# Kernel optimization log

Measured on AMD Instinct MI355X. Metric: run time of the kernel, lower is better.

## Reference

```python
import jax, jax.numpy as jnp
import numpy as np


def setup_inputs() -> dict:
    key = jax.random.key(0)
    ks = jax.random.split(key, 6)
    T, n_vars, n_channels, hidden = 2048, 64, 256, 512
    # VarianceScaling(2.0,'fan_in','uniform') ~ uniform(-limit, limit), limit=sqrt(3*2/fan_in)
    limit = float(np.sqrt(3.0 * 2.0 / n_channels))
    return {
        "enriched_history": jax.random.normal(ks[0], (T, n_vars, n_channels), dtype=jnp.float32),
        "target_mask": jax.random.randint(ks[1], (n_vars,), 0, 2, dtype=jnp.int32),
        "intervention_mask": jax.random.randint(ks[2], (n_vars,), 0, 2, dtype=jnp.int32),
        "W_target": jax.random.uniform(ks[3], (n_channels, hidden), jnp.float32, -limit, limit),
        "b_target": jnp.zeros((hidden,), jnp.float32),
        "W_intervention": jax.random.uniform(ks[4], (n_channels, hidden), jnp.float32, -limit, limit),
        "b_intervention": jnp.zeros((hidden,), jnp.float32),
        "W_other": jax.random.uniform(ks[5], (n_channels, hidden), jnp.float32, -limit, limit),
        "b_other": jnp.zeros((hidden,), jnp.float32),
    }


def reference(enriched_history, target_mask, intervention_mask,
              W_target, b_target, W_intervention, b_intervention,
              W_other, b_other):
    T, n_vars, n_channels = enriched_history.shape
    tm = target_mask.astype(jnp.float32)                       # [n_vars]
    im = intervention_mask.astype(jnp.float32) * (1.0 - tm)    # exclusivity
    om = (1.0 - tm) * (1.0 - im)

    flat = enriched_history.reshape(T * n_vars, n_channels)    # [T*n_vars, C]
    proj_t = flat @ W_target + b_target                        # [T*n_vars, H]
    proj_i = flat @ W_intervention + b_intervention
    proj_o = flat @ W_other + b_other

    # Faithful to original: jnp.repeat(mask, T) -> each variable's flag repeated T times
    tm_flat = jnp.repeat(tm, T)
    im_flat = jnp.repeat(im, T)
    om_flat = jnp.repeat(om, T)

    combined = (proj_t * tm_flat[:, None]
                + proj_i * im_flat[:, None]
                + proj_o * om_flat[:, None])
    return combined.reshape(T, n_vars, -1)
```

## Files before the change

### kernel.cpp

```cpp
#include <hip/hip_runtime.h>

typedef float f32x4 __attribute__((ext_vector_type(4)));
typedef unsigned short u16x8 __attribute__((ext_vector_type(8)));
typedef __bf16 bf16x8 __attribute__((ext_vector_type(8)));
typedef __bf16 bf16x4 __attribute__((ext_vector_type(4)));

__global__ __launch_bounds__(256) void convert_w_kernel(
    const float* __restrict__ Wt_, const float* __restrict__ Wi_,
    const float* __restrict__ Wo_, unsigned short* __restrict__ out)
{
    __shared__ unsigned short tile[64][72];

    const int b    = blockIdx.x;
    const int role = b >> 5;
    const int kt   = (b & 31) >> 3;
    const int nt   = b & 7;
    const float* __restrict__ W = (role == 0) ? Wt_ : ((role == 1) ? Wi_ : Wo_);

    const int t  = threadIdx.x;
    const int r0 = t >> 4;
    const int c4 = (t & 15) << 2;

#pragma unroll
    for (int j = 0; j < 4; ++j) {
        const int kl = r0 + j * 16;
        f32x4 v = *(const f32x4*)(W + (size_t)(kt * 64 + kl) * 512 + nt * 64 + c4);
#pragma unroll
        for (int e = 0; e < 4; ++e)
            tile[c4 + e][kl] = __builtin_bit_cast(unsigned short, (__bf16)v[e]);
    }
    __syncthreads();

    const int cs = t & 7;
#pragma unroll
    for (int p = 0; p < 2; ++p) {
        const int r = (t >> 3) + p * 32;
        u16x8 v = *(const u16x8*)&tile[r][cs * 8];
        *(u16x8*)(out + (size_t)role * 512 * 256 +
                  (size_t)(nt * 64 + r) * 256 + kt * 64 + cs * 8) = v;
    }
}

__global__ __launch_bounds__(512, 4) void role_proj_kernel(
    const float* __restrict__ A,
    const int* __restrict__ tmask,
    const int* __restrict__ imask,
    const unsigned short* __restrict__ Wws,
    const float* __restrict__ bt, const float* __restrict__ bi,
    const float* __restrict__ bo,
    float* __restrict__ C)
{
    __shared__ __align__(16) unsigned char smem[32 * 1024];
    unsigned short* As = (unsigned short*)smem;

    const int tid = threadIdx.x;
    const int m0  = blockIdx.x * 64;

    const int mi   = blockIdx.x >> 5;
    const int role = tmask[mi] ? 0 : (imask[mi] ? 1 : 2);
    const unsigned short* __restrict__ W = Wws + (size_t)role * (512 * 256);
    const float* __restrict__ bias = (role == 0) ? bt : ((role == 1) ? bi : bo);

    const f32x4* abase = (const f32x4*)(A + (size_t)m0 * 256);
    f32x4 ld[8];
#pragma unroll
    for (int p = 0; p < 8; ++p)
        ld[p] = __builtin_nontemporal_load(abase + tid + 512 * p);
#pragma unroll
    for (int p = 0; p < 8; ++p) {
        const int u    = tid + 512 * p;
        const int row  = u >> 6;
        const int slot = ((u & 63) >> 1) ^ (row & 7);
        bf16x4 pk = { (__bf16)ld[p][0], (__bf16)ld[p][1],
                      (__bf16)ld[p][2], (__bf16)ld[p][3] };
        *(bf16x4*)(smem + row * 512 + slot * 16 + (u & 1) * 8) = pk;
    }
    __syncthreads();

    const int lane  = tid & 63;
    const int wid   = tid >> 6;
    const int l15   = lane & 15;
    const int l4    = lane >> 4;
    const int nbase = wid * 64;
    const int r7    = l15 & 7;

    const unsigned short* wp[4];
#pragma unroll
    for (int fn = 0; fn < 4; ++fn)
        wp[fn] = W + (size_t)(nbase + fn * 16 + l15) * 256 + l4 * 8;

    f32x4 acc[4][4] = {};

#pragma unroll 1
    for (int ks = 0; ks < 8; ++ks) {
        u16x8 bfr[4];
#pragma unroll
        for (int fn = 0; fn < 4; ++fn)
            bfr[fn] = *(const u16x8*)(wp[fn] + ks * 32);
        u16x8 afr[4];
#pragma unroll
        for (int fm = 0; fm < 4; ++fm) {
            const int row  = fm * 16 + l15;
            const int slot = (ks * 4 + l4) ^ r7;
            afr[fm] = *(const u16x8*)&As[row * 256 + slot * 8];
        }
#pragma unroll
        for (int fm = 0; fm < 4; ++fm) {
#pragma unroll
            for (int fn = 0; fn < 4; ++fn) {
                acc[fm][fn] = __builtin_amdgcn_mfma_f32_16x16x32_bf16(
                    __builtin_bit_cast(bf16x8, bfr[fn]),
                    __builtin_bit_cast(bf16x8, afr[fm]),
                    acc[fm][fn], 0, 0, 0);
            }
        }
    }

    __builtin_amdgcn_sched_barrier(0);
    __builtin_amdgcn_s_barrier();
    __builtin_amdgcn_sched_barrier(0);

    f32x4 bv[4];
#pragma unroll
    for (int fn = 0; fn < 4; ++fn)
        bv[fn] = *(const f32x4*)(bias + nbase + fn * 16 + l4 * 4);

#pragma unroll
    for (int p = 0; p < 4; ++p) {
#pragma unroll
        for (int fn = 0; fn < 4; ++fn) {
            const int chunk = (wid * 16 + fn * 4 + l4) ^ r7;
            *(f32x4*)(smem + l15 * 2048 + chunk * 16) = acc[p][fn] + bv[fn];
        }
        asm volatile("s_waitcnt lgkmcnt(0)" ::: "memory");
        __builtin_amdgcn_sched_barrier(0);
        __builtin_amdgcn_s_barrier();
        __builtin_amdgcn_sched_barrier(0);

#pragma unroll
        for (int q = 0; q < 4; ++q) {
            const int f4    = tid + 512 * q;
            const int row   = f4 >> 7;
            const int chunk = f4 & 127;
            f32x4 v = *(const f32x4*)(smem + row * 2048 + (chunk ^ (row & 7)) * 16);
            __builtin_nontemporal_store(
                v, (f32x4*)(C + ((size_t)(m0 + p * 16 + row) << 9) + chunk * 4));
        }
        if (p < 3) {
            __builtin_amdgcn_sched_barrier(0);
            __builtin_amdgcn_s_barrier();
            __builtin_amdgcn_sched_barrier(0);
        }
    }
}

extern "C" void kernel_launch(void* const* d_in, const int* in_sizes, int n_in,
                              void* d_out, int out_size, void* d_ws, size_t ws_size,
                              hipStream_t stream) {
    const float* A   = (const float*)d_in[0];
    const int*   tm  = (const int*)d_in[1];
    const int*   im  = (const int*)d_in[2];
    const float* Wt_ = (const float*)d_in[3];
    const float* bt  = (const float*)d_in[4];
    const float* Wi_ = (const float*)d_in[5];
    const float* bi  = (const float*)d_in[6];
    const float* Wo_ = (const float*)d_in[7];
    const float* bo  = (const float*)d_in[8];

    unsigned short* Wws = (unsigned short*)d_ws;

    hipLaunchKernelGGL(convert_w_kernel, dim3(96), dim3(256),
                       0, stream, Wt_, Wi_, Wo_, Wws);

    hipLaunchKernelGGL(role_proj_kernel, dim3(2048), dim3(512),
                       0, stream, A, tm, im, Wws, bt, bi, bo, (float*)d_out);
}
```

Before: 123.2 us.

## Make projection blocks loop over four tiles with double-buffered A prefetch

Each block now processes four consecutive 64-row tiles instead of one, using a 2x32KB LDS double buffer. The next A tile's global loads are issued before the epilogue and converted into the other buffer afterwards, so input fetch overlaps with output writeback and MFMA work. The grid drops from 2048 to 512 blocks, and output stores become regular stores instead of nontemporal. The cost is doubled LDS per block, which limits how many blocks fit on a CU, plus extra barriers per iteration.

New measurement: 160.8 us. +30.5%, slower.

```diff
diff --git a/kernel.cpp b/kernel.cpp
--- a/kernel.cpp
+++ b/kernel.cpp
@@ -50,32 +50,15 @@
     const float* __restrict__ bo,
     float* __restrict__ C)
 {
-    __shared__ __align__(16) unsigned char smem[32 * 1024];
-    unsigned short* As = (unsigned short*)smem;
-
-    const int tid = threadIdx.x;
-    const int m0  = blockIdx.x * 64;
-
-    const int mi   = blockIdx.x >> 5;
+    __shared__ __align__(16) unsigned char smem[2][32 * 1024];
+
+    const int tid   = threadIdx.x;
+    const int tile0 = blockIdx.x * 4;
+
+    const int mi   = blockIdx.x >> 3;
     const int role = tmask[mi] ? 0 : (imask[mi] ? 1 : 2);
     const unsigned short* __restrict__ W = Wws + (size_t)role * (512 * 256);
     const float* __restrict__ bias = (role == 0) ? bt : ((role == 1) ? bi : bo);
-
-    const f32x4* abase = (const f32x4*)(A + (size_t)m0 * 256);
-    f32x4 ld[8];
-#pragma unroll
-    for (int p = 0; p < 8; ++p)
-        ld[p] = __builtin_nontemporal_load(abase + tid + 512 * p);
-#pragma unroll
-    for (int p = 0; p < 8; ++p) {
-        const int u    = tid + 512 * p;
-        const int row  = u >> 6;
-        const int slot = ((u & 63) >> 1) ^ (row & 7);
-        bf16x4 pk = { (__bf16)ld[p][0], (__bf16)ld[p][1],
-                      (__bf16)ld[p][2], (__bf16)ld[p][3] };
-        *(bf16x4*)(smem + row * 512 + slot * 16 + (u & 1) * 8) = pk;
-    }
-    __syncthreads();
 
     const int lane  = tid & 63;
     const int wid   = tid >> 6;
@@ -89,68 +72,120 @@
     for (int fn = 0; fn < 4; ++fn)
         wp[fn] = W + (size_t)(nbase + fn * 16 + l15) * 256 + l4 * 8;
 
-    f32x4 acc[4][4] = {};
-
+    {
+        const f32x4* abase = (const f32x4*)(A + (size_t)tile0 * 16384);
+        f32x4 ld[8];
+#pragma unroll
+        for (int p = 0; p < 8; ++p)
+            ld[p] = __builtin_nontemporal_load(abase + tid + 512 * p);
+#pragma unroll
+        for (int p = 0; p < 8; ++p) {
+            const int u    = tid + 512 * p;
+            const int row  = u >> 6;
+            const int slot = ((u & 63) >> 1) ^ (row & 7);
+            bf16x4 pk = { (__bf16)ld[p][0], (__bf16)ld[p][1],
+                          (__bf16)ld[p][2], (__bf16)ld[p][3] };
+            *(bf16x4*)(&smem[0][0] + row * 512 + slot * 16 + (u & 1) * 8) = pk;
+        }
+    }
+    __syncthreads();
+
+    int cur = 0;
 #pragma unroll 1
-    for (int ks = 0; ks < 8; ++ks) {
-        u16x8 bfr[4];
-#pragma unroll
-        for (int fn = 0; fn < 4; ++fn)
-            bfr[fn] = *(const u16x8*)(wp[fn] + ks * 32);
-        u16x8 afr[4];
-#pragma unroll
-        for (int fm = 0; fm < 4; ++fm) {
-            const int row  = fm * 16 + l15;
-            const int slot = (ks * 4 + l4) ^ r7;
-            afr[fm] = *(const u16x8*)&As[row * 256 + slot * 8];
-        }
-#pragma unroll
-        for (int fm = 0; fm < 4; ++fm) {
-#pragma unroll
-            for (int fn = 0; fn < 4; ++fn) {
-                acc[fm][fn] = __builtin_amdgcn_mfma_f32_16x16x32_bf16(
-                    __builtin_bit_cast(bf16x8, bfr[fn]),
-                    __builtin_bit_cast(bf16x8, afr[fm]),
-                    acc[fm][fn], 0, 0, 0);
-            }
-        }
-    }
-
-    __builtin_amdgcn_sched_barrier(0);
-    __builtin_amdgcn_s_barrier();
-    __builtin_amdgcn_sched_barrier(0);
-
-    f32x4 bv[4];
-#pragma unroll
-    for (int fn = 0; fn < 4; ++fn)
-        bv[fn] = *(const f32x4*)(bias + nbase + fn * 16 + l4 * 4);
-
-#pragma unroll
-    for (int p = 0; p < 4; ++p) {
-#pragma unroll
-        for (int fn = 0; fn < 4; ++fn) {
-            const int chunk = (wid * 16 + fn * 4 + l4) ^ r7;
-            *(f32x4*)(smem + l15 * 2048 + chunk * 16) = acc[p][fn] + bv[fn];
-        }
-        asm volatile("s_waitcnt lgkmcnt(0)" ::: "memory");
+    for (int it = 0; it < 4; ++it) {
+        const unsigned short* As = (const unsigned short*)&smem[cur][0];
+
+        f32x4 acc[4][4] = {};
+#pragma unroll 1
+        for (int ks = 0; ks < 8; ++ks) {
+            u16x8 bfr[4];
+#pragma unroll
+            for (int fn = 0; fn < 4; ++fn)
+                bfr[fn] = *(const u16x8*)(wp[fn] + ks * 32);
+            u16x8 afr[4];
+#pragma unroll
+            for (int fm = 0; fm < 4; ++fm) {
+                const int row  = fm * 16 + l15;
+                const int slot = (ks * 4 + l4) ^ r7;
+                afr[fm] = *(const u16x8*)&As[row * 256 + slot * 8];
+            }
+#pragma unroll
+            for (int fm = 0; fm < 4; ++fm) {
+#pragma unroll
+                for (int fn = 0; fn < 4; ++fn) {
+                    acc[fm][fn] = __builtin_amdgcn_mfma_f32_16x16x32_bf16(
+                        __builtin_bit_cast(bf16x8, bfr[fn]),
+                        __builtin_bit_cast(bf16x8, afr[fm]),
+                        acc[fm][fn], 0, 0, 0);
+                }
+            }
+        }
+
+        f32x4 ld[8];
+        if (it < 3) {
+            const f32x4* abase =
+                (const f32x4*)(A + (size_t)(tile0 + it + 1) * 16384);
+#pragma unroll
+            for (int p = 0; p < 8; ++p)
+                ld[p] = __builtin_nontemporal_load(abase + tid + 512 * p);
+        }
+
         __builtin_amdgcn_sched_barrier(0);
         __builtin_amdgcn_s_barrier();
         __builtin_amdgcn_sched_barrier(0);
 
-#pragma unroll
-        for (int q = 0; q < 4; ++q) {
-            const int f4    = tid + 512 * q;
-            const int row   = f4 >> 7;
-            const int chunk = f4 & 127;
-            f32x4 v = *(const f32x4*)(smem + row * 2048 + (chunk ^ (row & 7)) * 16);
-            __builtin_nontemporal_store(
-                v, (f32x4*)(C + ((size_t)(m0 + p * 16 + row) << 9) + chunk * 4));
-        }
-        if (p < 3) {
+        f32x4 bv[4];
+#pragma unroll
+        for (int fn = 0; fn < 4; ++fn)
+            bv[fn] = *(const f32x4*)(bias + nbase + fn * 16 + l4 * 4);
+
+        const int m0 = (tile0 + it) * 64;
+#pragma unroll
+        for (int p = 0; p < 4; ++p) {
+#pragma unroll
+            for (int fn = 0; fn < 4; ++fn) {
+                const int chunk = (wid * 16 + fn * 4 + l4) ^ r7;
+                *(f32x4*)(&smem[cur][0] + l15 * 2048 + chunk * 16) =
+                    acc[p][fn] + bv[fn];
+            }
+            asm volatile("s_waitcnt lgkmcnt(0)" ::: "memory");
             __builtin_amdgcn_sched_barrier(0);
             __builtin_amdgcn_s_barrier();
             __builtin_amdgcn_sched_barrier(0);
-        }
+
+#pragma unroll
+            for (int q = 0; q < 4; ++q) {
+                const int f4    = tid + 512 * q;
+                const int row   = f4 >> 7;
+                const int chunk = f4 & 127;
+                f32x4 v = *(const f32x4*)(&smem[cur][0] + row * 2048 +
+                                          ((chunk ^ (row & 7))) * 16);
+                *(f32x4*)(C + ((size_t)(m0 + p * 16 + row) << 9) + chunk * 4) = v;
+            }
+            if (p < 3) {
+                __builtin_amdgcn_sched_barrier(0);
+                __builtin_amdgcn_s_barrier();
+                __builtin_amdgcn_sched_barrier(0);
+            }
+        }
+
+        if (it < 3) {
+#pragma unroll
+            for (int p = 0; p < 8; ++p) {
+                const int u    = tid + 512 * p;
+                const int row  = u >> 6;
+                const int slot = ((u & 63) >> 1) ^ (row & 7);
+                bf16x4 pk = { (__bf16)ld[p][0], (__bf16)ld[p][1],
+                              (__bf16)ld[p][2], (__bf16)ld[p][3] };
+                *(bf16x4*)(&smem[cur ^ 1][0] + row * 512 + slot * 16 +
+                           (u & 1) * 8) = pk;
+            }
+            asm volatile("s_waitcnt lgkmcnt(0)" ::: "memory");
+            __builtin_amdgcn_sched_barrier(0);
+            __builtin_amdgcn_s_barrier();
+            __builtin_amdgcn_sched_barrier(0);
+        }
+        cur ^= 1;
     }
 }
 
@@ -172,6 +207,6 @@
     hipLaunchKernelGGL(convert_w_kernel, dim3(96), dim3(256),
                        0, stream, Wt_, Wi_, Wo_, Wws);
 
-    hipLaunchKernelGGL(role_proj_kernel, dim3(2048), dim3(512),
+    hipLaunchKernelGGL(role_proj_kernel, dim3(512), dim3(512),
                        0, stream, A, tm, im, Wws, bt, bi, bo, (float*)d_out);
 }
```
